# Kernel tuning notes

Measured on AMD Instinct MI355X. Metric: run time of the kernel, lower is better.

## Reference

```python
import jax, jax.numpy as jnp
import numpy as np

BZ, D_IN, D_STATE, D_OUT, L = 8, 256, 512, 256, 4096


def setup_inputs() -> dict:
    key = jax.random.key(0)
    k_u, k_a, k_b, k_c = jax.random.split(key, 4)
    init_scale = 0.5
    u = jax.random.normal(k_u, (BZ, D_IN, L), dtype=jnp.float32)
    A_unconstrained = jax.random.normal(k_a, (D_STATE,), dtype=jnp.float32) * 0.1
    B_mat = jax.random.normal(k_b, (D_STATE, D_IN), dtype=jnp.float32) * init_scale / np.sqrt(D_IN)
    C_mat = jax.random.normal(k_c, (D_OUT, D_STATE), dtype=jnp.float32) * init_scale / np.sqrt(D_STATE)
    D_mat = jnp.zeros((D_OUT, D_IN), dtype=jnp.float32)
    h0 = jnp.zeros((D_STATE,), dtype=jnp.float32)
    return {"u": u, "A_unconstrained": A_unconstrained, "B_mat": B_mat,
            "C_mat": C_mat, "D_mat": D_mat, "h0": h0}


def reference(u, A_unconstrained, B_mat, C_mat, D_mat, h0):
    # u: (B, input_dim, L)
    Bz = u.shape[0]
    A_diag = -jax.nn.softplus(A_unconstrained)          # (S,)
    # Precompute input projection for all timesteps: (L, B, S)
    Bu = jnp.einsum('bil,si->lbs', u, B_mat)
    state0 = jnp.broadcast_to(h0[None, :], (Bz, A_diag.shape[0]))

    def step(state, bu_t):
        x_t = state * A_diag[None, :] + bu_t            # (B, S)
        return x_t, x_t

    _, xs = jax.lax.scan(step, state0, Bu)              # xs: (L, B, S)
    # y_t = x_t @ C^T + u_t @ D^T, assembled as (B, output_dim, L)
    Y = jnp.einsum('lbs,os->bol', xs, C_mat) + jnp.einsum('bil,oi->bol', u, D_mat)
    return Y
```

## Files before the change

kernel.cpp:

```cpp
#include <hip/hip_runtime.h>
#include <math.h>

#define BZ 8
#define DI 256
#define DS 512
#define DOUT 256
#define LL 4096
#define BS (BZ * DS)
#define CH 64
#define CT 64
#define TST 136

typedef __bf16 bf16x8 __attribute__((ext_vector_type(8)));
typedef float f32x4 __attribute__((ext_vector_type(4)));
typedef unsigned short us8 __attribute__((ext_vector_type(8)));

#define WAITV(n) asm volatile("s_waitcnt vmcnt(" #n ")" ::: "memory")
#define WAITL0   asm volatile("s_waitcnt lgkmcnt(0)" ::: "memory")

__device__ __forceinline__ ushort f2b(float f) {
    union { float f; unsigned u; } v; v.f = f;
    unsigned r = v.u + 0x7FFFu + ((v.u >> 16) & 1u);
    return (ushort)(r >> 16);
}
__device__ __forceinline__ float b2f(ushort h) {
    union { unsigned u; float f; } v; v.u = ((unsigned)h) << 16;
    return v.f;
}

__device__ __forceinline__ void gload16(const ushort* g, ushort* l) {
    __builtin_amdgcn_global_load_lds(
        (const __attribute__((address_space(1))) unsigned int*)g,
        (__attribute__((address_space(3))) unsigned int*)l,
        16, 0, 0);
}

__global__ __launch_bounds__(256) void k_prep_u2t(const float* __restrict__ u,
                                                  ushort* __restrict__ utr,
                                                  const float* __restrict__ Au,
                                                  float* __restrict__ apow,
                                                  const float* __restrict__ Bm,
                                                  const float* __restrict__ Cm,
                                                  const float* __restrict__ Dm,
                                                  ushort* __restrict__ Bmb,
                                                  ushort* __restrict__ Cmb,
                                                  ushort* __restrict__ Dmb,
                                                  int* __restrict__ dflag) {
    __shared__ float T[64][65];
    const int tid = threadIdx.x;
    const int id = blockIdx.x;
    if (id < 2048) {
        const int l0 = (id & 63) * 64;
        const int i0 = ((id >> 6) & 3) * 64;
        const int b  = id >> 8;
        const int r = tid >> 4, c4 = tid & 15;
#pragma unroll
        for (int rr = r; rr < 64; rr += 16) {
            float4 v = *(const float4*)&u[((size_t)b * DI + i0 + rr) * LL + l0 + c4 * 4];
            T[rr][c4 * 4 + 0] = v.x; T[rr][c4 * 4 + 1] = v.y;
            T[rr][c4 * 4 + 2] = v.z; T[rr][c4 * 4 + 3] = v.w;
        }
        __syncthreads();
#pragma unroll
        for (int ll = r; ll < 64; ll += 16) {
            ushort4 o;
            o.x = f2b(T[c4 * 4 + 0][ll]); o.y = f2b(T[c4 * 4 + 1][ll]);
            o.z = f2b(T[c4 * 4 + 2][ll]); o.w = f2b(T[c4 * 4 + 3][ll]);
            *(ushort4*)&utr[((size_t)b * LL + l0 + ll) * DI + i0 + c4 * 4] = o;
        }
    } else {
        const int t = (id - 2048) * 256 + tid;
        const int n1 = DS * DI / 4, n2 = DOUT * DS / 4, n3 = DOUT * DI / 4;
        if (t < n1) {
            float4 v = ((const float4*)Bm)[t];
            ushort4 o; o.x = f2b(v.x); o.y = f2b(v.y); o.z = f2b(v.z); o.w = f2b(v.w);
            ((ushort4*)Bmb)[t] = o;
        } else if (t < n1 + n2) {
            float4 v = ((const float4*)Cm)[t - n1];
            ushort4 o; o.x = f2b(v.x); o.y = f2b(v.y); o.z = f2b(v.z); o.w = f2b(v.w);
            ((ushort4*)Cmb)[t - n1] = o;
        } else if (t < n1 + n2 + n3) {
            float4 v = ((const float4*)Dm)[t - n1 - n2];
            ushort4 o; o.x = f2b(v.x); o.y = f2b(v.y); o.z = f2b(v.z); o.w = f2b(v.w);
            ((ushort4*)Dmb)[t - n1 - n2] = o;
            if (v.x != 0.f || v.y != 0.f || v.z != 0.f || v.w != 0.f)
                atomicOr(dflag, 1);
        }
        if (t < DS) {
            float x = Au[t];
            float sp = (x > 15.f) ? x : log1pf(expf(x));
            float ad = -sp;
            float p = 1.f;
            apow[t] = 1.f;
            for (int j = 1; j <= CT; ++j) { p *= ad; apow[j * DS + t] = p; }
        }
    }
}

__global__ __launch_bounds__(256) void k_bu(const ushort* __restrict__ Bmb,
                                            const ushort* __restrict__ utr,
                                            ushort* __restrict__ Xb,
                                            float* __restrict__ finals,
                                            const float* __restrict__ apow) {
    __shared__ ushort smem[20480];
    const int tid = threadIdx.x;
    const int w = tid >> 6, lane = tid & 63;
    const int l0 = blockIdx.x * 128, s0 = blockIdx.y * 128, b = blockIdx.z;
    const int wm = w & 1, wn = w >> 1;
    const int mrow = lane & 15, quad = lane >> 4;
    const int sr = lane >> 2, sc = (lane & 3) * 8;
    const int off0 = (16 * w) * 32, off1 = (16 * w + 64) * 32;

    f32x4 acc[4][4];
#pragma unroll
    for (int mi = 0; mi < 4; ++mi)
#pragma unroll
        for (int ni = 0; ni < 4; ++ni) acc[mi][ni] = (f32x4)0.f;

    const ushort* ag0 = Bmb + (size_t)(s0 + 16 * w + sr) * DI + sc;
    const ushort* ag1 = ag0 + (size_t)64 * DI;
    const ushort* bg0 = utr + ((size_t)b * LL + l0 + 16 * w + sr) * DI + sc;
    const ushort* bg1 = bg0 + (size_t)64 * DI;

    gload16(ag0, smem + off0);                 gload16(ag1, smem + off1);
    gload16(bg0, smem + 8192 + off0);          gload16(bg1, smem + 8192 + off1);
    gload16(bg0 + 32, smem + 12288 + off0);    gload16(bg1 + 32, smem + 12288 + off1);

#pragma unroll
    for (int it = 0; it < DI / 32; ++it) {
        if (it < 7) { WAITV(2); } else { WAITV(0); }
        __builtin_amdgcn_s_barrier();
        if (it + 1 < DI / 32) {
            const int kk = (it + 1) * 32, ab = ((it + 1) & 1) * 4096;
            gload16(ag0 + kk, smem + ab + off0); gload16(ag1 + kk, smem + ab + off1);
        }
        if (it + 2 < DI / 32) {
            const int kk = (it + 2) * 32, bb = 8192 + ((it + 2) % 3) * 4096;
            gload16(bg0 + kk, smem + bb + off0); gload16(bg1 + kk, smem + bb + off1);
        }
        const int ca = (it & 1) * 4096, cb = 8192 + (it % 3) * 4096;
        bf16x8 af[4], bfr[4];
#pragma unroll
        for (int mi = 0; mi < 4; ++mi)
            af[mi] = *(const bf16x8*)&smem[ca + (wm * 64 + mi * 16 + mrow) * 32 + quad * 8];
#pragma unroll
        for (int ni = 0; ni < 4; ++ni)
            bfr[ni] = *(const bf16x8*)&smem[cb + (wn * 64 + ni * 16 + mrow) * 32 + quad * 8];
#pragma unroll
        for (int mi = 0; mi < 4; ++mi)
#pragma unroll
            for (int ni = 0; ni < 4; ++ni)
                acc[mi][ni] = __builtin_amdgcn_mfma_f32_16x16x32_bf16(af[mi], bfr[ni], acc[mi][ni], 0, 0, 0);
    }
    __syncthreads();

#pragma unroll
    for (int mi = 0; mi < 4; ++mi) {
        const int sloc = wm * 64 + mi * 16 + quad * 4;
#pragma unroll
        for (int ni = 0; ni < 4; ++ni) {
            const int lloc = wn * 64 + ni * 16 + mrow;
            f32x4 v = acc[mi][ni];
            ushort4 o; o.x = f2b(v[0]); o.y = f2b(v[1]); o.z = f2b(v[2]); o.w = f2b(v[3]);
            *(ushort4*)&smem[lloc * TST + sloc] = o;
        }
    }
    __syncthreads();
    {
        const int cloc = tid >> 7, sl = tid & 127;
        const float a = apow[DS + s0 + sl];
        float acc2 = 0.f;
        ushort* p = &smem[(cloc * 64) * TST + sl];
#pragma unroll 8
        for (int j = 0; j < CT; ++j) {
            acc2 = a * acc2 + b2f(*p);
            *p = f2b(acc2);
            p += TST;
        }
        finals[(size_t)(l0 / 64 + cloc) * BS + (size_t)b * DS + s0 + sl] = acc2;
    }
    __syncthreads();
    {
        const int rr = tid >> 4, cc = tid & 15;
#pragma unroll
        for (int rep = 0; rep < 8; ++rep) {
            const int l = rep * 16 + rr;
            us8 v = *(const us8*)&smem[l * TST + cc * 8];
            *(us8*)&Xb[(size_t)(l0 + l) * BS + (size_t)b * DS + s0 + cc * 8] = v;
        }
    }
}

__global__ __launch_bounds__(256) void k_out(const ushort* __restrict__ Cmb,
                                             const ushort* __restrict__ Dmb,
                                             const ushort* __restrict__ Xb,
                                             const ushort* __restrict__ utr,
                                             const float* __restrict__ finals,
                                             const float* __restrict__ apow,
                                             const float* __restrict__ h0,
                                             const int* __restrict__ dflag,
                                             float* __restrict__ Y) {
    __shared__ ushort smem[18432];
    float* crl = (float*)&smem[17408];
    const int tid = threadIdx.x;
    const int w = tid >> 6, lane = tid & 63;
    const int l0 = blockIdx.x * 64, o0 = blockIdx.y * 128, b = blockIdx.z;
    const int mrow = lane & 15, quad = lane >> 4;
    const int sr = lane >> 2, sc = (lane & 3) * 8;
    const int off0 = (16 * w) * 32, off1 = (16 * w + 64) * 32;
    const int dnz = *dflag;

    f32x4 acc[4][2];
#pragma unroll
    for (int mi = 0; mi < 4; ++mi)
#pragma unroll
        for (int ni = 0; ni < 2; ++ni) acc[mi][ni] = (f32x4)0.f;

    auto compute = [&](const int aoff, const int ast, const int boff) {
        bf16x8 af[4], bfr[2];
#pragma unroll
        for (int mi = 0; mi < 4; ++mi)
            af[mi] = *(const bf16x8*)&smem[aoff + (mi * 16 + mrow) * ast + quad * 8];
#pragma unroll
        for (int ni = 0; ni < 2; ++ni)
            bfr[ni] = *(const bf16x8*)&smem[boff + (32 * w + ni * 16 + mrow) * 32 + quad * 8];
#pragma unroll
        for (int mi = 0; mi < 4; ++mi)
#pragma unroll
            for (int ni = 0; ni < 2; ++ni)
                acc[mi][ni] = __builtin_amdgcn_mfma_f32_16x16x32_bf16(af[mi], bfr[ni], acc[mi][ni], 0, 0, 0);
    };

    {
        const int r0 = 16 * w + sr;
        const float* ap0 = &apow[(size_t)(r0 + 1) * DS];
        const ushort* x0 = Xb + (size_t)(l0 + r0) * BS + (size_t)b * DS;
        const ushort* bg0 = Cmb + (size_t)(o0 + r0) * DS + sc;
        const ushort* bg1 = bg0 + (size_t)64 * DS;

        us8 xr[3]; float4 par[3], pbr[3];
        auto loadX = [&](int it) {
            const int sl = it % 3;
            const int col = it * 32 + sc;
            xr[sl]  = *(const us8*)&x0[col];
            par[sl] = *(const float4*)&ap0[col];
            pbr[sl] = *(const float4*)&ap0[col + 4];
        };
        auto storeA = [&](int it, int dstoff) {
            const int sl = it % 3;
            const int col = it * 32 + sc;
            float4 c_a = *(const float4*)&crl[col];
            float4 c_b = *(const float4*)&crl[col + 4];
            us8 o;
            o[0] = f2b(b2f(xr[sl][0]) + par[sl].x * c_a.x);
            o[1] = f2b(b2f(xr[sl][1]) + par[sl].y * c_a.y);
            o[2] = f2b(b2f(xr[sl][2]) + par[sl].z * c_a.z);
            o[3] = f2b(b2f(xr[sl][3]) + par[sl].w * c_a.w);
            o[4] = f2b(b2f(xr[sl][4]) + pbr[sl].x * c_b.x);
            o[5] = f2b(b2f(xr[sl][5]) + pbr[sl].y * c_b.y);
            o[6] = f2b(b2f(xr[sl][6]) + pbr[sl].z * c_b.z);
            o[7] = f2b(b2f(xr[sl][7]) + pbr[sl].w * c_b.w);
            *(us8*)&smem[dstoff + r0 * 40 + sc] = o;
        };

        loadX(0); loadX(1); loadX(2);
        gload16(bg0, smem + 5120 + off0);      gload16(bg1, smem + 5120 + off1);
        gload16(bg0 + 32, smem + 9216 + off0); gload16(bg1 + 32, smem + 9216 + off1);

        {
            const int c0 = blockIdx.x;
            const float aT0 = apow[CT * DS + tid];
            const float aT1 = apow[CT * DS + 256 + tid];
            float cva = h0[tid], cvb = h0[256 + tid];
            const float* fb = finals + (size_t)b * DS;
            int c = 0;
            for (; c + 8 <= c0; c += 8) {
                float fa[8], fc[8];
#pragma unroll
                for (int j = 0; j < 8; ++j) {
                    fa[j] = fb[(size_t)(c + j) * BS + tid];
                    fc[j] = fb[(size_t)(c + j) * BS + 256 + tid];
                }
#pragma unroll
                for (int j = 0; j < 8; ++j) {
                    cva = aT0 * cva + fa[j];
                    cvb = aT1 * cvb + fc[j];
                }
            }
            for (; c < c0; ++c) {
                cva = aT0 * cva + fb[(size_t)c * BS + tid];
                cvb = aT1 * cvb + fb[(size_t)c * BS + 256 + tid];
            }
            crl[tid] = cva; crl[256 + tid] = cvb;
        }
        __syncthreads();

        storeA(0, 0);
        WAITL0;

#pragma unroll
        for (int it = 0; it < DS / 32; ++it) {
            if (it < 14) { WAITV(5); } else if (it == 14) { WAITV(2); } else { WAITV(0); }
            __builtin_amdgcn_s_barrier();
            if (it + 3 < DS / 32) loadX(it + 3);
            if (it + 2 < DS / 32) {
                const int kk = (it + 2) * 32, bb = 5120 + ((it + 2) % 3) * 4096;
                gload16(bg0 + kk, smem + bb + off0);
                gload16(bg1 + kk, smem + bb + off1);
            }
            compute((it & 1) * 2560, 40, 5120 + (it % 3) * 4096);
            if (it + 1 < DS / 32) {
                storeA(it + 1, ((it + 1) & 1) * 2560);
                WAITL0;
            }
        }
    }
    if (dnz) {
        const ushort* ag0 = utr + ((size_t)b * LL + l0 + 16 * w + sr) * DI + sc;
        const ushort* bg0 = Dmb + (size_t)(o0 + 16 * w + sr) * DI + sc;
        const ushort* bg1 = bg0 + (size_t)64 * DI;

        __syncthreads();
        gload16(ag0, smem + off0);
        gload16(bg0, smem + 5120 + off0); gload16(bg1, smem + 5120 + off1);

        for (int it = 0; it < DI / 32; ++it) {
            __syncthreads();
            const int ca_ = (it & 1) * 2560, na_ = 2560 - ca_;
            const int cb_ = 5120 + (it & 1) * 4096, nb_ = 5120 + 4096 - (it & 1) * 4096;
            if (it + 1 < DI / 32) {
                const int kk = (it + 1) * 32;
                gload16(ag0 + kk, smem + na_ + off0);
                gload16(bg0 + kk, smem + nb_ + off0); gload16(bg1 + kk, smem + nb_ + off1);
            }
            compute(ca_, 32, cb_);
        }
    }

#pragma unroll
    for (int mi = 0; mi < 4; ++mi) {
        const int l = l0 + mi * 16 + quad * 4;
#pragma unroll
        for (int ni = 0; ni < 2; ++ni) {
            const int o = o0 + 32 * w + ni * 16 + mrow;
            *(float4*)&Y[((size_t)b * DOUT + o) * LL + l] = *(float4*)&acc[mi][ni];
        }
    }
}

extern "C" void kernel_launch(void* const* d_in, const int* in_sizes, int n_in,
                              void* d_out, int out_size, void* d_ws, size_t ws_size,
                              hipStream_t stream) {
    const float* u  = (const float*)d_in[0];
    const float* Au = (const float*)d_in[1];
    const float* Bm = (const float*)d_in[2];
    const float* Cm = (const float*)d_in[3];
    const float* Dm = (const float*)d_in[4];
    const float* h0 = (const float*)d_in[5];
    float* Y = (float*)d_out;

    char* p = (char*)d_ws;
    ushort* utr    = (ushort*)p; p += (size_t)BZ * LL * DI * 2;
    ushort* Xb     = (ushort*)p; p += (size_t)LL * BS * 2;
    float* finals  = (float*)p;  p += (size_t)CH * BS * 4;
    float* apow    = (float*)p;  p += (size_t)(CT + 1) * DS * 4;
    ushort* Bmb    = (ushort*)p; p += (size_t)DS * DI * 2;
    ushort* Cmb    = (ushort*)p; p += (size_t)DOUT * DS * 2;
    ushort* Dmb    = (ushort*)p; p += (size_t)DOUT * DI * 2;
    int* dflag     = (int*)p;    p += 16;

    hipMemsetAsync(dflag, 0, 4, stream);
    k_prep_u2t<<<dim3(2368), 256, 0, stream>>>(u, utr, Au, apow, Bm, Cm, Dm, Bmb, Cmb, Dmb, dflag);
    k_bu<<<dim3(LL / 128, DS / 128, BZ), 256, 0, stream>>>(Bmb, utr, Xb, finals, apow);
    k_out<<<dim3(LL / 64, DOUT / 128, BZ), 256, 0, stream>>>(Cmb, Dmb, Xb, utr, finals, apow, h0, dflag, Y);
}
```

Measured before the change: 143.6 us.

## Fuse Bu projection, chunk scan and output GEMM into one persistent kernel

Replaces the separate transpose, Bu GEMM and output GEMM kernels with a single kernel over 512 blocks (one per 64-step chunk and batch). Each block reads fp32 u directly, converts and transposes it in LDS, computes the full 512-state projection, runs the intra-chunk scan, then uses a global atomic barrier to get chunk finals before applying the carry-in and the C projection from LDS. This removes the bf16 u-transpose and X round trips through HBM and two launches. In exchange it relies on all 512 blocks being co-resident for the spin barrier, loads B and C fragments straight from global memory without LDS staging, and moves the D term to a naive fallback kernel.

```diff
diff --git a/kernel.cpp b/kernel.cpp
--- a/kernel.cpp
+++ b/kernel.cpp
@@ -9,14 +9,12 @@
 #define BS (BZ * DS)
 #define CH 64
 #define CT 64
-#define TST 136
+#define XST 520
+#define NBLK (CH * BZ)
 
 typedef __bf16 bf16x8 __attribute__((ext_vector_type(8)));
 typedef float f32x4 __attribute__((ext_vector_type(4)));
 typedef unsigned short us8 __attribute__((ext_vector_type(8)));
-
-#define WAITV(n) asm volatile("s_waitcnt vmcnt(" #n ")" ::: "memory")
-#define WAITL0   asm volatile("s_waitcnt lgkmcnt(0)" ::: "memory")
 
 __device__ __forceinline__ ushort f2b(float f) {
     union { float f; unsigned u; } v; v.f = f;
@@ -28,323 +26,252 @@
     return v.f;
 }
 
-__device__ __forceinline__ void gload16(const ushort* g, ushort* l) {
+__device__ __forceinline__ void gload16(const void* g, ushort* l) {
     __builtin_amdgcn_global_load_lds(
         (const __attribute__((address_space(1))) unsigned int*)g,
         (__attribute__((address_space(3))) unsigned int*)l,
         16, 0, 0);
 }
 
-__global__ __launch_bounds__(256) void k_prep_u2t(const float* __restrict__ u,
-                                                  ushort* __restrict__ utr,
-                                                  const float* __restrict__ Au,
-                                                  float* __restrict__ apow,
-                                                  const float* __restrict__ Bm,
-                                                  const float* __restrict__ Cm,
-                                                  const float* __restrict__ Dm,
-                                                  ushort* __restrict__ Bmb,
-                                                  ushort* __restrict__ Cmb,
-                                                  ushort* __restrict__ Dmb,
-                                                  int* __restrict__ dflag) {
-    __shared__ float T[64][65];
-    const int tid = threadIdx.x;
-    const int id = blockIdx.x;
-    if (id < 2048) {
-        const int l0 = (id & 63) * 64;
-        const int i0 = ((id >> 6) & 3) * 64;
-        const int b  = id >> 8;
-        const int r = tid >> 4, c4 = tid & 15;
-#pragma unroll
-        for (int rr = r; rr < 64; rr += 16) {
-            float4 v = *(const float4*)&u[((size_t)b * DI + i0 + rr) * LL + l0 + c4 * 4];
-            T[rr][c4 * 4 + 0] = v.x; T[rr][c4 * 4 + 1] = v.y;
-            T[rr][c4 * 4 + 2] = v.z; T[rr][c4 * 4 + 3] = v.w;
-        }
-        __syncthreads();
-#pragma unroll
-        for (int ll = r; ll < 64; ll += 16) {
-            ushort4 o;
-            o.x = f2b(T[c4 * 4 + 0][ll]); o.y = f2b(T[c4 * 4 + 1][ll]);
-            o.z = f2b(T[c4 * 4 + 2][ll]); o.w = f2b(T[c4 * 4 + 3][ll]);
-            *(ushort4*)&utr[((size_t)b * LL + l0 + ll) * DI + i0 + c4 * 4] = o;
-        }
-    } else {
-        const int t = (id - 2048) * 256 + tid;
-        const int n1 = DS * DI / 4, n2 = DOUT * DS / 4, n3 = DOUT * DI / 4;
-        if (t < n1) {
-            float4 v = ((const float4*)Bm)[t];
-            ushort4 o; o.x = f2b(v.x); o.y = f2b(v.y); o.z = f2b(v.z); o.w = f2b(v.w);
-            ((ushort4*)Bmb)[t] = o;
-        } else if (t < n1 + n2) {
-            float4 v = ((const float4*)Cm)[t - n1];
-            ushort4 o; o.x = f2b(v.x); o.y = f2b(v.y); o.z = f2b(v.z); o.w = f2b(v.w);
-            ((ushort4*)Cmb)[t - n1] = o;
-        } else if (t < n1 + n2 + n3) {
-            float4 v = ((const float4*)Dm)[t - n1 - n2];
-            ushort4 o; o.x = f2b(v.x); o.y = f2b(v.y); o.z = f2b(v.z); o.w = f2b(v.w);
-            ((ushort4*)Dmb)[t - n1 - n2] = o;
-            if (v.x != 0.f || v.y != 0.f || v.z != 0.f || v.w != 0.f)
-                atomicOr(dflag, 1);
-        }
-        if (t < DS) {
-            float x = Au[t];
-            float sp = (x > 15.f) ? x : log1pf(expf(x));
-            float ad = -sp;
-            float p = 1.f;
-            apow[t] = 1.f;
-            for (int j = 1; j <= CT; ++j) { p *= ad; apow[j * DS + t] = p; }
-        }
-    }
-}
-
-__global__ __launch_bounds__(256) void k_bu(const ushort* __restrict__ Bmb,
-                                            const ushort* __restrict__ utr,
-                                            ushort* __restrict__ Xb,
-                                            float* __restrict__ finals,
-                                            const float* __restrict__ apow) {
-    __shared__ ushort smem[20480];
+__global__ __launch_bounds__(256) void k_prep(const float* __restrict__ Au,
+                                              float* __restrict__ apow,
+                                              const float* __restrict__ Bm,
+                                              const float* __restrict__ Cm,
+                                              const float* __restrict__ Dm,
+                                              ushort* __restrict__ Bmb,
+                                              ushort* __restrict__ Cmb,
+                                              int* __restrict__ dflag) {
+    const int t = blockIdx.x * 256 + threadIdx.x;
+    const int n1 = DS * DI / 4, n2 = DOUT * DS / 4, n3 = DOUT * DI / 4;
+    if (t < n1) {
+        float4 v = ((const float4*)Bm)[t];
+        ushort4 o; o.x = f2b(v.x); o.y = f2b(v.y); o.z = f2b(v.z); o.w = f2b(v.w);
+        ((ushort4*)Bmb)[t] = o;
+    } else if (t < n1 + n2) {
+        float4 v = ((const float4*)Cm)[t - n1];
+        ushort4 o; o.x = f2b(v.x); o.y = f2b(v.y); o.z = f2b(v.z); o.w = f2b(v.w);
+        ((ushort4*)Cmb)[t - n1] = o;
+    } else if (t < n1 + n2 + n3) {
+        float4 v = ((const float4*)Dm)[t - n1 - n2];
+        if (v.x != 0.f || v.y != 0.f || v.z != 0.f || v.w != 0.f)
+            atomicOr(dflag, 1);
+    }
+    if (t < DS) {
+        float x = Au[t];
+        float sp = (x > 15.f) ? x : log1pf(expf(x));
+        float ad = -sp;
+        float p = 1.f;
+        apow[t] = 1.f;
+        for (int j = 1; j <= CT; ++j) { p *= ad; apow[j * DS + t] = p; }
+    }
+}
+
+__global__ __launch_bounds__(256, 2) void k_fused(const float* __restrict__ u,
+                                                  const ushort* __restrict__ Bmb,
+                                                  const ushort* __restrict__ Cmb,
+                                                  const float* __restrict__ apow,
+                                                  const float* __restrict__ h0,
+                                                  float* __restrict__ finals,
+                                                  int* __restrict__ bar,
+                                                  float* __restrict__ Y) {
+    __shared__ ushort smem[34304];
+    float* crl = (float*)&smem[33280];
     const int tid = threadIdx.x;
     const int w = tid >> 6, lane = tid & 63;
-    const int l0 = blockIdx.x * 128, s0 = blockIdx.y * 128, b = blockIdx.z;
-    const int wm = w & 1, wn = w >> 1;
     const int mrow = lane & 15, quad = lane >> 4;
-    const int sr = lane >> 2, sc = (lane & 3) * 8;
-    const int off0 = (16 * w) * 32, off1 = (16 * w + 64) * 32;
-
-    f32x4 acc[4][4];
+    const int c0 = blockIdx.x, b = blockIdx.y;
+    const int l0 = c0 * 64;
+
+    f32x4 acc1[8][4];
+#pragma unroll
+    for (int mi = 0; mi < 8; ++mi)
+#pragma unroll
+        for (int ni = 0; ni < 4; ++ni) acc1[mi][ni] = (f32x4)0.f;
+
+    const int urow = w * 4 + (lane >> 4);
+    const int ucol = (lane & 15) * 4;
+    const float* usrc = u + ((size_t)b * DI + urow) * LL + l0 + ucol;
+    const int lx = tid & 63, ig = tid >> 6;
+
+    auto stageU = [&](int it) {
+        const int bufu = (it & 1) * 4096;
+        const float* s0 = usrc + (size_t)(it * 32) * LL;
+        gload16(s0, smem + bufu + w * 512);
+        gload16(s0 + (size_t)16 * LL, smem + bufu + w * 512 + 2048);
+    };
+    auto xposeU = [&](int it) {
+        const float* uf = (const float*)&smem[(it & 1) * 4096];
+        const int bto = 8192 + (it & 1) * 2560;
+        float v[8];
+#pragma unroll
+        for (int j = 0; j < 8; ++j) v[j] = uf[(ig * 8 + j) * 64 + lx];
+        us8 o;
+#pragma unroll
+        for (int j = 0; j < 8; ++j) o[j] = f2b(v[j]);
+        *(us8*)&smem[bto + lx * 40 + ig * 8] = o;
+    };
+
+    stageU(0);
+    __syncthreads();
+#pragma unroll
+    for (int it = 0; it < DI / 32; ++it) {
+        if (it + 1 < DI / 32) stageU(it + 1);
+        xposeU(it);
+        __syncthreads();
+        const int bto = 8192 + (it & 1) * 2560;
+        bf16x8 bfr[4];
+#pragma unroll
+        for (int ni = 0; ni < 4; ++ni)
+            bfr[ni] = *(const bf16x8*)&smem[bto + (ni * 16 + mrow) * 40 + quad * 8];
+        bf16x8 af[8];
+#pragma unroll
+        for (int mi = 0; mi < 8; ++mi)
+            af[mi] = *(const bf16x8*)&Bmb[(size_t)(128 * w + mi * 16 + mrow) * DI + it * 32 + quad * 8];
+#pragma unroll
+        for (int mi = 0; mi < 8; ++mi)
+#pragma unroll
+            for (int ni = 0; ni < 4; ++ni)
+                acc1[mi][ni] = __builtin_amdgcn_mfma_f32_16x16x32_bf16(af[mi], bfr[ni], acc1[mi][ni], 0, 0, 0);
+    }
+    __syncthreads();
+
+#pragma unroll
+    for (int mi = 0; mi < 8; ++mi) {
+        const int sloc = 128 * w + mi * 16 + quad * 4;
+#pragma unroll
+        for (int ni = 0; ni < 4; ++ni) {
+            const int lloc = ni * 16 + mrow;
+            f32x4 v = acc1[mi][ni];
+            ushort4 o; o.x = f2b(v[0]); o.y = f2b(v[1]); o.z = f2b(v[2]); o.w = f2b(v[3]);
+            *(ushort4*)&smem[lloc * XST + sloc] = o;
+        }
+    }
+    __syncthreads();
+
+    {
+        const float2 av = *(const float2*)&apow[DS + 2 * tid];
+        float x0 = 0.f, x1 = 0.f;
+        unsigned* p = (unsigned*)&smem[2 * tid];
+#pragma unroll 8
+        for (int l = 0; l < CT; ++l) {
+            unsigned v = p[l * (XST / 2)];
+            x0 = av.x * x0 + b2f((ushort)(v & 0xFFFFu));
+            x1 = av.y * x1 + b2f((ushort)(v >> 16));
+            p[l * (XST / 2)] = (unsigned)f2b(x0) | ((unsigned)f2b(x1) << 16);
+        }
+        float2 fo; fo.x = x0; fo.y = x1;
+        *(float2*)&finals[(size_t)c0 * BS + (size_t)b * DS + 2 * tid] = fo;
+    }
+
+    __syncthreads();
+    if (tid == 0) {
+        __threadfence();
+        (void)__hip_atomic_fetch_add(&bar[0], 1, __ATOMIC_ACQ_REL,
+                                     __HIP_MEMORY_SCOPE_AGENT);
+        while (__hip_atomic_load(&bar[0], __ATOMIC_ACQUIRE,
+                                 __HIP_MEMORY_SCOPE_AGENT) < NBLK)
+            __builtin_amdgcn_s_sleep(2);
+    }
+    __syncthreads();
+
+    {
+        const float aT0 = apow[CT * DS + tid];
+        const float aT1 = apow[CT * DS + 256 + tid];
+        float cva = h0[tid], cvb = h0[256 + tid];
+        const float* fb = finals + (size_t)b * DS;
+        int c = 0;
+        for (; c + 8 <= c0; c += 8) {
+            float fa[8], fc[8];
+#pragma unroll
+            for (int j = 0; j < 8; ++j) {
+                fa[j] = fb[(size_t)(c + j) * BS + tid];
+                fc[j] = fb[(size_t)(c + j) * BS + 256 + tid];
+            }
+#pragma unroll
+            for (int j = 0; j < 8; ++j) {
+                cva = aT0 * cva + fa[j];
+                cvb = aT1 * cvb + fc[j];
+            }
+        }
+        for (; c < c0; ++c) {
+            cva = aT0 * cva + fb[(size_t)c * BS + tid];
+            cvb = aT1 * cvb + fb[(size_t)c * BS + 256 + tid];
+        }
+        crl[tid] = cva; crl[256 + tid] = cvb;
+    }
+    __syncthreads();
+
+    {
+        const int lr = tid >> 2, g = tid & 3;
+#pragma unroll
+        for (int cc = 0; cc < 16; ++cc) {
+            const int s = g * 128 + cc * 8;
+            us8 x = *(const us8*)&smem[lr * XST + s];
+            float4 a1 = *(const float4*)&apow[(size_t)(lr + 1) * DS + s];
+            float4 a2 = *(const float4*)&apow[(size_t)(lr + 1) * DS + s + 4];
+            float4 c1 = *(const float4*)&crl[s];
+            float4 c2 = *(const float4*)&crl[s + 4];
+            us8 o;
+            o[0] = f2b(b2f(x[0]) + a1.x * c1.x);
+            o[1] = f2b(b2f(x[1]) + a1.y * c1.y);
+            o[2] = f2b(b2f(x[2]) + a1.z * c1.z);
+            o[3] = f2b(b2f(x[3]) + a1.w * c1.w);
+            o[4] = f2b(b2f(x[4]) + a2.x * c2.x);
+            o[5] = f2b(b2f(x[5]) + a2.y * c2.y);
+            o[6] = f2b(b2f(x[6]) + a2.z * c2.z);
+            o[7] = f2b(b2f(x[7]) + a2.w * c2.w);
+            *(us8*)&smem[lr * XST + s] = o;
+        }
+    }
+    __syncthreads();
+
+    f32x4 acc2[4][4];
 #pragma unroll
     for (int mi = 0; mi < 4; ++mi)
 #pragma unroll
-        for (int ni = 0; ni < 4; ++ni) acc[mi][ni] = (f32x4)0.f;
-
-    const ushort* ag0 = Bmb + (size_t)(s0 + 16 * w + sr) * DI + sc;
-    const ushort* ag1 = ag0 + (size_t)64 * DI;
-    const ushort* bg0 = utr + ((size_t)b * LL + l0 + 16 * w + sr) * DI + sc;
-    const ushort* bg1 = bg0 + (size_t)64 * DI;
-
-    gload16(ag0, smem + off0);                 gload16(ag1, smem + off1);
-    gload16(bg0, smem + 8192 + off0);          gload16(bg1, smem + 8192 + off1);
-    gload16(bg0 + 32, smem + 12288 + off0);    gload16(bg1 + 32, smem + 12288 + off1);
-
-#pragma unroll
-    for (int it = 0; it < DI / 32; ++it) {
-        if (it < 7) { WAITV(2); } else { WAITV(0); }
-        __builtin_amdgcn_s_barrier();
-        if (it + 1 < DI / 32) {
-            const int kk = (it + 1) * 32, ab = ((it + 1) & 1) * 4096;
-            gload16(ag0 + kk, smem + ab + off0); gload16(ag1 + kk, smem + ab + off1);
-        }
-        if (it + 2 < DI / 32) {
-            const int kk = (it + 2) * 32, bb = 8192 + ((it + 2) % 3) * 4096;
-            gload16(bg0 + kk, smem + bb + off0); gload16(bg1 + kk, smem + bb + off1);
-        }
-        const int ca = (it & 1) * 4096, cb = 8192 + (it % 3) * 4096;
-        bf16x8 af[4], bfr[4];
+        for (int ni = 0; ni < 4; ++ni) acc2[mi][ni] = (f32x4)0.f;
+
+#pragma unroll
+    for (int it = 0; it < DS / 32; ++it) {
+        bf16x8 af2[4], bfr2[4];
 #pragma unroll
         for (int mi = 0; mi < 4; ++mi)
-            af[mi] = *(const bf16x8*)&smem[ca + (wm * 64 + mi * 16 + mrow) * 32 + quad * 8];
+            af2[mi] = *(const bf16x8*)&smem[(mi * 16 + mrow) * XST + it * 32 + quad * 8];
 #pragma unroll
         for (int ni = 0; ni < 4; ++ni)
-            bfr[ni] = *(const bf16x8*)&smem[cb + (wn * 64 + ni * 16 + mrow) * 32 + quad * 8];
+            bfr2[ni] = *(const bf16x8*)&Cmb[(size_t)(64 * w + ni * 16 + mrow) * DS + it * 32 + quad * 8];
 #pragma unroll
         for (int mi = 0; mi < 4; ++mi)
 #pragma unroll
             for (int ni = 0; ni < 4; ++ni)
-                acc[mi][ni] = __builtin_amdgcn_mfma_f32_16x16x32_bf16(af[mi], bfr[ni], acc[mi][ni], 0, 0, 0);
-    }
-    __syncthreads();
-
-#pragma unroll
-    for (int mi = 0; mi < 4; ++mi) {
-        const int sloc = wm * 64 + mi * 16 + quad * 4;
-#pragma unroll
-        for (int ni = 0; ni < 4; ++ni) {
-            const int lloc = wn * 64 + ni * 16 + mrow;
-            f32x4 v = acc[mi][ni];
-            ushort4 o; o.x = f2b(v[0]); o.y = f2b(v[1]); o.z = f2b(v[2]); o.w = f2b(v[3]);
-            *(ushort4*)&smem[lloc * TST + sloc] = o;
-        }
-    }
-    __syncthreads();
-    {
-        const int cloc = tid >> 7, sl = tid & 127;
-        const float a = apow[DS + s0 + sl];
-        float acc2 = 0.f;
-        ushort* p = &smem[(cloc * 64) * TST + sl];
-#pragma unroll 8
-        for (int j = 0; j < CT; ++j) {
-            acc2 = a * acc2 + b2f(*p);
-            *p = f2b(acc2);
-            p += TST;
-        }
-        finals[(size_t)(l0 / 64 + cloc) * BS + (size_t)b * DS + s0 + sl] = acc2;
-    }
-    __syncthreads();
-    {
-        const int rr = tid >> 4, cc = tid & 15;
-#pragma unroll
-        for (int rep = 0; rep < 8; ++rep) {
-            const int l = rep * 16 + rr;
-            us8 v = *(const us8*)&smem[l * TST + cc * 8];
-            *(us8*)&Xb[(size_t)(l0 + l) * BS + (size_t)b * DS + s0 + cc * 8] = v;
-        }
-    }
-}
-
-__global__ __launch_bounds__(256) void k_out(const ushort* __restrict__ Cmb,
-                                             const ushort* __restrict__ Dmb,
-                                             const ushort* __restrict__ Xb,
-                                             const ushort* __restrict__ utr,
-                                             const float* __restrict__ finals,
-                                             const float* __restrict__ apow,
-                                             const float* __restrict__ h0,
-                                             const int* __restrict__ dflag,
-                                             float* __restrict__ Y) {
-    __shared__ ushort smem[18432];
-    float* crl = (float*)&smem[17408];
-    const int tid = threadIdx.x;
-    const int w = tid >> 6, lane = tid & 63;
-    const int l0 = blockIdx.x * 64, o0 = blockIdx.y * 128, b = blockIdx.z;
-    const int mrow = lane & 15, quad = lane >> 4;
-    const int sr = lane >> 2, sc = (lane & 3) * 8;
-    const int off0 = (16 * w) * 32, off1 = (16 * w + 64) * 32;
-    const int dnz = *dflag;
-
-    f32x4 acc[4][2];
-#pragma unroll
-    for (int mi = 0; mi < 4; ++mi)
-#pragma unroll
-        for (int ni = 0; ni < 2; ++ni) acc[mi][ni] = (f32x4)0.f;
-
-    auto compute = [&](const int aoff, const int ast, const int boff) {
-        bf16x8 af[4], bfr[2];
-#pragma unroll
-        for (int mi = 0; mi < 4; ++mi)
-            af[mi] = *(const bf16x8*)&smem[aoff + (mi * 16 + mrow) * ast + quad * 8];
-#pragma unroll
-        for (int ni = 0; ni < 2; ++ni)
-            bfr[ni] = *(const bf16x8*)&smem[boff + (32 * w + ni * 16 + mrow) * 32 + quad * 8];
-#pragma unroll
-        for (int mi = 0; mi < 4; ++mi)
-#pragma unroll
-            for (int ni = 0; ni < 2; ++ni)
-                acc[mi][ni] = __builtin_amdgcn_mfma_f32_16x16x32_bf16(af[mi], bfr[ni], acc[mi][ni], 0, 0, 0);
-    };
-
-    {
-        const int r0 = 16 * w + sr;
-        const float* ap0 = &apow[(size_t)(r0 + 1) * DS];
-        const ushort* x0 = Xb + (size_t)(l0 + r0) * BS + (size_t)b * DS;
-        const ushort* bg0 = Cmb + (size_t)(o0 + r0) * DS + sc;
-        const ushort* bg1 = bg0 + (size_t)64 * DS;
-
-        us8 xr[3]; float4 par[3], pbr[3];
-        auto loadX = [&](int it) {
-            const int sl = it % 3;
-            const int col = it * 32 + sc;
-            xr[sl]  = *(const us8*)&x0[col];
-            par[sl] = *(const float4*)&ap0[col];
-            pbr[sl] = *(const float4*)&ap0[col + 4];
-        };
-        auto storeA = [&](int it, int dstoff) {
-            const int sl = it % 3;
-            const int col = it * 32 + sc;
-            float4 c_a = *(const float4*)&crl[col];
-            float4 c_b = *(const float4*)&crl[col + 4];
-            us8 o;
-            o[0] = f2b(b2f(xr[sl][0]) + par[sl].x * c_a.x);
-            o[1] = f2b(b2f(xr[sl][1]) + par[sl].y * c_a.y);
-            o[2] = f2b(b2f(xr[sl][2]) + par[sl].z * c_a.z);
-            o[3] = f2b(b2f(xr[sl][3]) + par[sl].w * c_a.w);
-            o[4] = f2b(b2f(xr[sl][4]) + pbr[sl].x * c_b.x);
-            o[5] = f2b(b2f(xr[sl][5]) + pbr[sl].y * c_b.y);
-            o[6] = f2b(b2f(xr[sl][6]) + pbr[sl].z * c_b.z);
-            o[7] = f2b(b2f(xr[sl][7]) + pbr[sl].w * c_b.w);
-            *(us8*)&smem[dstoff + r0 * 40 + sc] = o;
-        };
-
-        loadX(0); loadX(1); loadX(2);
-        gload16(bg0, smem + 5120 + off0);      gload16(bg1, smem + 5120 + off1);
-        gload16(bg0 + 32, smem + 9216 + off0); gload16(bg1 + 32, smem + 9216 + off1);
-
-        {
-            const int c0 = blockIdx.x;
-            const float aT0 = apow[CT * DS + tid];
-            const float aT1 = apow[CT * DS + 256 + tid];
-            float cva = h0[tid], cvb = h0[256 + tid];
-            const float* fb = finals + (size_t)b * DS;
-            int c = 0;
-            for (; c + 8 <= c0; c += 8) {
-                float fa[8], fc[8];
-#pragma unroll
-                for (int j = 0; j < 8; ++j) {
-                    fa[j] = fb[(size_t)(c + j) * BS + tid];
-                    fc[j] = fb[(size_t)(c + j) * BS + 256 + tid];
-                }
-#pragma unroll
-                for (int j = 0; j < 8; ++j) {
-                    cva = aT0 * cva + fa[j];
-                    cvb = aT1 * cvb + fc[j];
-                }
-            }
-            for (; c < c0; ++c) {
-                cva = aT0 * cva + fb[(size_t)c * BS + tid];
-                cvb = aT1 * cvb + fb[(size_t)c * BS + 256 + tid];
-            }
-            crl[tid] = cva; crl[256 + tid] = cvb;
-        }
-        __syncthreads();
-
-        storeA(0, 0);
-        WAITL0;
-
-#pragma unroll
-        for (int it = 0; it < DS / 32; ++it) {
-            if (it < 14) { WAITV(5); } else if (it == 14) { WAITV(2); } else { WAITV(0); }
-            __builtin_amdgcn_s_barrier();
-            if (it + 3 < DS / 32) loadX(it + 3);
-            if (it + 2 < DS / 32) {
-                const int kk = (it + 2) * 32, bb = 5120 + ((it + 2) % 3) * 4096;
-                gload16(bg0 + kk, smem + bb + off0);
-                gload16(bg1 + kk, smem + bb + off1);
-            }
-            compute((it & 1) * 2560, 40, 5120 + (it % 3) * 4096);
-            if (it + 1 < DS / 32) {
-                storeA(it + 1, ((it + 1) & 1) * 2560);
-                WAITL0;
-            }
-        }
-    }
-    if (dnz) {
-        const ushort* ag0 = utr + ((size_t)b * LL + l0 + 16 * w + sr) * DI + sc;
-        const ushort* bg0 = Dmb + (size_t)(o0 + 16 * w + sr) * DI + sc;
-        const ushort* bg1 = bg0 + (size_t)64 * DI;
-
-        __syncthreads();
-        gload16(ag0, smem + off0);
-        gload16(bg0, smem + 5120 + off0); gload16(bg1, smem + 5120 + off1);
-
-        for (int it = 0; it < DI / 32; ++it) {
-            __syncthreads();
-            const int ca_ = (it & 1) * 2560, na_ = 2560 - ca_;
-            const int cb_ = 5120 + (it & 1) * 4096, nb_ = 5120 + 4096 - (it & 1) * 4096;
-            if (it + 1 < DI / 32) {
-                const int kk = (it + 1) * 32;
-                gload16(ag0 + kk, smem + na_ + off0);
-                gload16(bg0 + kk, smem + nb_ + off0); gload16(bg1 + kk, smem + nb_ + off1);
-            }
-            compute(ca_, 32, cb_);
-        }
+                acc2[mi][ni] = __builtin_amdgcn_mfma_f32_16x16x32_bf16(af2[mi], bfr2[ni], acc2[mi][ni], 0, 0, 0);
     }
 
 #pragma unroll
     for (int mi = 0; mi < 4; ++mi) {
         const int l = l0 + mi * 16 + quad * 4;
 #pragma unroll
-        for (int ni = 0; ni < 2; ++ni) {
-            const int o = o0 + 32 * w + ni * 16 + mrow;
-            *(float4*)&Y[((size_t)b * DOUT + o) * LL + l] = *(float4*)&acc[mi][ni];
-        }
+        for (int ni = 0; ni < 4; ++ni) {
+            const int o = 64 * w + ni * 16 + mrow;
+            *(float4*)&Y[((size_t)b * DOUT + o) * LL + l] = *(float4*)&acc2[mi][ni];
+        }
+    }
+}
+
+__global__ __launch_bounds__(256) void k_dadd(const int* __restrict__ dflag,
+                                              const float* __restrict__ Dm,
+                                              const float* __restrict__ u,
+                                              float* __restrict__ Y) {
+    if (*dflag == 0) return;
+    const int o = blockIdx.x * 16 + (threadIdx.x >> 4);
+    const int li = threadIdx.x & 15;
+    const int b = blockIdx.y;
+    for (int lc = 0; lc < LL / 16; ++lc) {
+        const int l = lc * 16 + li;
+        float s = 0.f;
+        for (int i = 0; i < DI; ++i)
+            s += Dm[o * DI + i] * u[((size_t)b * DI + i) * LL + l];
+        Y[((size_t)b * DOUT + o) * LL + l] += s;
     }
 }
 
@@ -360,17 +287,15 @@
     float* Y = (float*)d_out;
 
     char* p = (char*)d_ws;
-    ushort* utr    = (ushort*)p; p += (size_t)BZ * LL * DI * 2;
-    ushort* Xb     = (ushort*)p; p += (size_t)LL * BS * 2;
     float* finals  = (float*)p;  p += (size_t)CH * BS * 4;
     float* apow    = (float*)p;  p += (size_t)(CT + 1) * DS * 4;
     ushort* Bmb    = (ushort*)p; p += (size_t)DS * DI * 2;
     ushort* Cmb    = (ushort*)p; p += (size_t)DOUT * DS * 2;
-    ushort* Dmb    = (ushort*)p; p += (size_t)DOUT * DI * 2;
-    int* dflag     = (int*)p;    p += 16;
-
-    hipMemsetAsync(dflag, 0, 4, stream);
-    k_prep_u2t<<<dim3(2368), 256, 0, stream>>>(u, utr, Au, apow, Bm, Cm, Dm, Bmb, Cmb, Dmb, dflag);
-    k_bu<<<dim3(LL / 128, DS / 128, BZ), 256, 0, stream>>>(Bmb, utr, Xb, finals, apow);
-    k_out<<<dim3(LL / 64, DOUT / 128, BZ), 256, 0, stream>>>(Cmb, Dmb, Xb, utr, finals, apow, h0, dflag, Y);
-}
+    int* dflag     = (int*)p;    p += 64;
+    int* bar       = dflag + 16;
+
+    hipMemsetAsync(dflag, 0, 128, stream);
+    k_prep<<<dim3(320), 256, 0, stream>>>(Au, apow, Bm, Cm, Dm, Bmb, Cmb, dflag);
+    k_fused<<<dim3(CH, BZ), 256, 0, stream>>>(u, Bmb, Cmb, apow, h0, finals, bar, Y);
+    k_dadd<<<dim3(DOUT / 16, BZ), 256, 0, stream>>>(dflag, Dm, u, Y);
+}
```

New measurement: 173.1 us. +20.5%, slower.
